# Performance work log

Measured on AMD Instinct MI355X. Metric: run time of the kernel, lower is better.

The kernel has to match this reference:

```python
import jax, jax.numpy as jnp
import numpy as np

N_NODES = 50000
N_EDGES = 800000
IN_CH, HID, OUT_CH = 3, 64, 768
NEG_SLOPE = 0.01  # torch LeakyReLU default
BN_EPS = 1e-5


def _gcn_conv(x, edge_index, W, b):
    # PyG GCNConv: add self-loops, symmetric degree normalization, scatter-add.
    n = x.shape[0]
    loops = jnp.arange(n, dtype=edge_index.dtype)
    src = jnp.concatenate([edge_index[0], loops])
    dst = jnp.concatenate([edge_index[1], loops])
    deg = jax.ops.segment_sum(jnp.ones(src.shape[0], x.dtype), dst, num_segments=n)
    dinv = jnp.where(deg > 0, jax.lax.rsqrt(deg), 0.0)
    norm = dinv[src] * dinv[dst]                      # [E+N]
    h = x @ W                                          # [N, out]
    msg = h[src] * norm[:, None]                       # gather + edge scale
    return jax.ops.segment_sum(msg, dst, num_segments=n) + b


def _block(x, edge_index, W, b, gamma, beta):
    h = _gcn_conv(x, edge_index, W, b)
    h = jnp.where(h >= 0, h, NEG_SLOPE * h)            # LeakyReLU
    mean = h.mean(axis=0)
    var = h.var(axis=0)                                # biased, as torch BN train
    h = (h - mean) * jax.lax.rsqrt(var + BN_EPS) * gamma + beta
    return h                                           # dropout: identity (eval)


def _glorot(key, fan_in, fan_out):
    s = np.sqrt(6.0 / (fan_in + fan_out)).astype(np.float32)
    return jax.random.uniform(key, (fan_in, fan_out), jnp.float32, -s, s)


def setup_inputs() -> dict:
    key = jax.random.key(0)
    ks = jax.random.split(key, 8)
    x = jax.random.normal(ks[0], (N_NODES, IN_CH), jnp.float32)
    edge_index = jax.random.randint(ks[1], (2, N_EDGES), 0, N_NODES, jnp.int64)
    inp = {"x": x, "edge_index": edge_index}
    inp["W1"] = _glorot(ks[2], IN_CH, HID)
    inp["b1"] = jnp.zeros((HID,), jnp.float32)
    inp["g1"] = jnp.ones((HID,), jnp.float32)
    inp["be1"] = jnp.zeros((HID,), jnp.float32)
    inp["W2"] = _glorot(ks[3], HID, HID)
    inp["b2"] = jnp.zeros((HID,), jnp.float32)
    inp["g2"] = jnp.ones((HID,), jnp.float32)
    inp["be2"] = jnp.zeros((HID,), jnp.float32)
    inp["W3"] = _glorot(ks[4], HID, HID)
    inp["b3"] = jnp.zeros((HID,), jnp.float32)
    inp["g3"] = jnp.ones((HID,), jnp.float32)
    inp["be3"] = jnp.zeros((HID,), jnp.float32)
    inp["Wmu"] = _glorot(ks[5], HID, OUT_CH)
    inp["bmu"] = jnp.zeros((OUT_CH,), jnp.float32)
    inp["Wls"] = _glorot(ks[6], HID, OUT_CH)
    inp["bls"] = jnp.zeros((OUT_CH,), jnp.float32)
    return inp


def reference(x, edge_index, W1, b1, g1, be1, W2, b2, g2, be2, W3, b3, g3, be3, Wmu, bmu, Wls, bls):
    h = _block(x, edge_index, W1, b1, g1, be1)
    h = _block(h, edge_index, W2, b2, g2, be2)
    h = _block(h, edge_index, W3, b3, g3, be3)
    mu = _gcn_conv(h, edge_index, Wmu, bmu)
    logstd = _gcn_conv(h, edge_index, Wls, bls)
    return (mu, logstd)
```

## Files before the change

### kernel.cpp

```cpp
#include <hip/hip_runtime.h>
#include <cstddef>


#define NEG_SLOPE 0.01f
#define BN_EPS 1e-5f

typedef unsigned short u16;
typedef __attribute__((ext_vector_type(8))) short bf16x8;
typedef __attribute__((ext_vector_type(4))) float f32x4;

__device__ __forceinline__ unsigned bf16_rne(float x) {
  unsigned u = __float_as_uint(x);
  return (u + 0x7fffu + ((u >> 16) & 1u)) >> 16;
}

__global__ __launch_bounds__(256) void init_k(int* __restrict__ cnt,
                                              float* __restrict__ bns, int N) {
  int i = blockIdx.x * 256 + threadIdx.x;
  if (i < N) cnt[i] = 0;
  if (i < 384) bns[i] = 0.0f;
}

__global__ __launch_bounds__(256) void hist_k(const int* __restrict__ dst,
                                              int* __restrict__ cnt, int E) {
  int e = blockIdx.x * 256 + threadIdx.x;
  if (e < E) atomicAdd(&cnt[dst[e]], 1);
}

__global__ __launch_bounds__(1024) void scanA(const int* __restrict__ cnt,
                                              int* __restrict__ pre,
                                              int* __restrict__ bsum, int N) {
  __shared__ int sh[1024];
  const int t = threadIdx.x;
  const int i = blockIdx.x * 1024 + t;
  int c = (i < N) ? cnt[i] : 0;
  sh[t] = c;
  __syncthreads();
  for (int off = 1; off < 1024; off <<= 1) {
    int v = (t >= off) ? sh[t - off] : 0;
    __syncthreads();
    sh[t] += v;
    __syncthreads();
  }
  if (i < N) pre[i] = sh[t] - c;
  if (t == 1023) bsum[blockIdx.x] = sh[t];
}

__global__ __launch_bounds__(64) void scanB(int* __restrict__ bsum, int nb) {
  int t = threadIdx.x;
  int orig = (t < nb) ? bsum[t] : 0;
  int v = orig;
#pragma unroll
  for (int off = 1; off < 64; off <<= 1) {
    int u = __shfl_up(v, off);
    if (t >= off) v += u;
  }
  if (t < nb) bsum[t] = v - orig;
}

__global__ __launch_bounds__(256) void scanC(const int* __restrict__ cnt,
                                             int* __restrict__ rowptr,
                                             int* __restrict__ cursor,
                                             const int* __restrict__ bsum,
                                             float* __restrict__ dinv,
                                             int N, int E) {
  int i = blockIdx.x * 256 + threadIdx.x;
  if (i < N) {
    int rp = rowptr[i] + bsum[i >> 10];
    rowptr[i] = rp;
    cursor[i] = rp;
    dinv[i] = rsqrtf((float)(cnt[i] + 1));
  }
  if (i == 0) rowptr[N] = E;
}

__global__ __launch_bounds__(256) void fill_k(const int* __restrict__ src,
                                              const int* __restrict__ dst,
                                              int* __restrict__ cursor,
                                              int* __restrict__ eidx, int E) {
  int e = blockIdx.x * 256 + threadIdx.x;
  if (e >= E) return;
  int p = atomicAdd(&cursor[dst[e]], 1);
  eidx[p] = src[e];
}

__global__ __launch_bounds__(256) void l1_fused(
    const int* __restrict__ rowptr, const int* __restrict__ eidx,
    const float* __restrict__ x, const float* __restrict__ dinv,
    const float* __restrict__ W1, const float* __restrict__ b1,
    float* __restrict__ Z, float* __restrict__ q, float* __restrict__ bns, int N) {
  const int t = threadIdx.x, lane = t & 63, wid = t >> 6;
  const int gw = blockIdx.x * 4 + wid;
  const int nw = gridDim.x * 4;
  const float w0 = W1[lane], w1 = W1[64 + lane], w2 = W1[128 + lane];
  const float bb = b1[lane];
  float s1 = 0.f, s2 = 0.f;
  for (int node = gw; node < N; node += nw) {
    int beg = rowptr[node], end = rowptr[node + 1];
    float a0 = 0.f, a1 = 0.f, a2 = 0.f, aq = 0.f;
    for (int e = beg + lane; e < end; e += 64) {
      int s = eidx[e];
      float dv = dinv[s];
      a0 += x[s * 3] * dv;
      a1 += x[s * 3 + 1] * dv;
      a2 += x[s * 3 + 2] * dv;
      aq += dv;
    }
#pragma unroll
    for (int off = 32; off; off >>= 1) {
      a0 += __shfl_xor(a0, off);
      a1 += __shfl_xor(a1, off);
      a2 += __shfl_xor(a2, off);
      aq += __shfl_xor(aq, off);
    }
    float dv = dinv[node];
    a0 += x[node * 3] * dv;
    a1 += x[node * 3 + 1] * dv;
    a2 += x[node * 3 + 2] * dv;
    aq += dv;
    float u = dv * (a0 * w0 + a1 * w1 + a2 * w2) + bb;
    float o = u >= 0.f ? u : NEG_SLOPE * u;
    Z[(size_t)node * 64 + lane] = o * dv;
    s1 += o;
    s2 += o * o;
    if (lane == 0) q[node] = aq;
  }
  __shared__ float red[8][64];
  red[wid][lane] = s1;
  red[4 + wid][lane] = s2;
  __syncthreads();
  if (t < 64) {
    atomicAdd(&bns[t], red[0][t] + red[1][t] + red[2][t] + red[3][t]);
    atomicAdd(&bns[64 + t], red[4][t] + red[5][t] + red[6][t] + red[7][t]);
  }
}

__global__ __launch_bounds__(256) void gather64(const int* __restrict__ rowptr,
                                                const int* __restrict__ eidx,
                                                const float* __restrict__ Z,
                                                float* __restrict__ G, int N) {
  int node = blockIdx.x * 4 + (threadIdx.x >> 6);
  if (node >= N) return;
  int lane = threadIdx.x & 63;
  int slot = lane >> 4;
  int c4 = (lane & 15) << 2;
  int beg = rowptr[node], end = rowptr[node + 1];
  float ax = 0.f, ay = 0.f, az = 0.f, aw = 0.f;
  int e = beg + slot;
  for (; e + 4 < end; e += 8) {
    int s0 = eidx[e], s1 = eidx[e + 4];
    float4 v0 = *(const float4*)(Z + (size_t)s0 * 64 + c4);
    float4 v1 = *(const float4*)(Z + (size_t)s1 * 64 + c4);
    ax += v0.x + v1.x;
    ay += v0.y + v1.y;
    az += v0.z + v1.z;
    aw += v0.w + v1.w;
  }
  if (e < end) {
    int s0 = eidx[e];
    float4 v0 = *(const float4*)(Z + (size_t)s0 * 64 + c4);
    ax += v0.x; ay += v0.y; az += v0.z; aw += v0.w;
  }
#pragma unroll
  for (int off = 16; off < 64; off <<= 1) {
    ax += __shfl_xor(ax, off);
    ay += __shfl_xor(ay, off);
    az += __shfl_xor(az, off);
    aw += __shfl_xor(aw, off);
  }
  if (slot == 0) {
    float4 self = *(const float4*)(Z + (size_t)node * 64 + c4);
    float4 o = make_float4(ax + self.x, ay + self.y, az + self.z, aw + self.w);
    *(float4*)(G + (size_t)node * 64 + c4) = o;
  }
}

__global__ __launch_bounds__(256) void gather64h(const int* __restrict__ rowptr,
                                                 const int* __restrict__ eidx,
                                                 const float* __restrict__ Z,
                                                 u16* __restrict__ Ghi,
                                                 u16* __restrict__ Glo, int N) {
  int node = blockIdx.x * 4 + (threadIdx.x >> 6);
  if (node >= N) return;
  int lane = threadIdx.x & 63;
  int slot = lane >> 4;
  int c4 = (lane & 15) << 2;
  int beg = rowptr[node], end = rowptr[node + 1];
  float ax = 0.f, ay = 0.f, az = 0.f, aw = 0.f;
  int e = beg + slot;
  for (; e + 4 < end; e += 8) {
    int s0 = eidx[e], s1 = eidx[e + 4];
    float4 v0 = *(const float4*)(Z + (size_t)s0 * 64 + c4);
    float4 v1 = *(const float4*)(Z + (size_t)s1 * 64 + c4);
    ax += v0.x + v1.x;
    ay += v0.y + v1.y;
    az += v0.z + v1.z;
    aw += v0.w + v1.w;
  }
  if (e < end) {
    int s0 = eidx[e];
    float4 v0 = *(const float4*)(Z + (size_t)s0 * 64 + c4);
    ax += v0.x; ay += v0.y; az += v0.z; aw += v0.w;
  }
#pragma unroll
  for (int off = 16; off < 64; off <<= 1) {
    ax += __shfl_xor(ax, off);
    ay += __shfl_xor(ay, off);
    az += __shfl_xor(az, off);
    aw += __shfl_xor(aw, off);
  }
  if (slot == 0) {
    float4 self = *(const float4*)(Z + (size_t)node * 64 + c4);
    float o0 = ax + self.x, o1 = ay + self.y, o2 = az + self.z, o3 = aw + self.w;
    unsigned h0 = bf16_rne(o0), h1 = bf16_rne(o1), h2 = bf16_rne(o2), h3 = bf16_rne(o3);
    unsigned l0 = bf16_rne(o0 - __uint_as_float(h0 << 16));
    unsigned l1 = bf16_rne(o1 - __uint_as_float(h1 << 16));
    unsigned l2 = bf16_rne(o2 - __uint_as_float(h2 << 16));
    unsigned l3 = bf16_rne(o3 - __uint_as_float(h3 << 16));
    uint2 hv = make_uint2(h0 | (h1 << 16), h2 | (h3 << 16));
    uint2 lv = make_uint2(l0 | (l1 << 16), l2 | (l3 << 16));
    *(uint2*)(Ghi + (size_t)node * 64 + c4) = hv;
    *(uint2*)(Glo + (size_t)node * 64 + c4) = lv;
  }
}

__global__ __launch_bounds__(256) void prep_small(
    const float* __restrict__ bns, const float* __restrict__ g,
    const float* __restrict__ be, const float* __restrict__ W,
    float* __restrict__ Wc, float* __restrict__ cx, float invN) {
  __shared__ float sc[64], sh[64], part[4][64];
  int t = threadIdx.x;
  if (t < 64) {
    float mean = bns[t] * invN;
    float var = bns[64 + t] * invN - mean * mean;
    float s = g[t] * rsqrtf(var + BN_EPS);
    sc[t] = s;
    sh[t] = be[t] - mean * s;
  }
  __syncthreads();
  int c = t & 63, kq = t >> 6;
  float p = 0.f;
  for (int k = kq * 16; k < kq * 16 + 16; ++k) {
    float w = W[k * 64 + c];
    Wc[k * 64 + c] = sc[k] * w;
    p += sh[k] * w;
  }
  part[kq][c] = p;
  __syncthreads();
  if (t < 64) cx[t] = part[0][t] + part[1][t] + part[2][t] + part[3][t];
}

__global__ __launch_bounds__(256) void prep_head(
    const float* __restrict__ bns, const float* __restrict__ g,
    const float* __restrict__ be, const float* __restrict__ Wmu,
    const float* __restrict__ Wls, u16* __restrict__ Bh, u16* __restrict__ Bl,
    float* __restrict__ cmu, float* __restrict__ cls, float invN) {
  __shared__ float sc[64], sh[64], part[2][128];
  int t = threadIdx.x;
  if (t < 64) {
    float mean = bns[t] * invN;
    float var = bns[64 + t] * invN - mean * mean;
    float s = g[t] * rsqrtf(var + BN_EPS);
    sc[t] = s;
    sh[t] = be[t] - mean * s;
  }
  __syncthreads();
  int blk = blockIdx.x;
  int head = blk >= 6 ? 1 : 0;
  int cc = head ? blk - 6 : blk;
  int c0 = cc * 128;
  const float* W = head ? Wls : Wmu;
  float* cx = head ? cls : cmu;
  int cl = t & 127, kh = t >> 7;
  int c = c0 + cl;
  int ct = cl >> 4, jc = cl & 15;
  size_t base = (size_t)(head * 6 + cc) * 2 * 8 * 64 * 8;
  float p = 0.f;
  for (int k = kh * 32; k < kh * 32 + 32; ++k) {
    float w = W[(size_t)k * 768 + c];
    float wc = sc[k] * w;
    p += sh[k] * w;
    unsigned hi = bf16_rne(wc);
    unsigned lo = bf16_rne(wc - __uint_as_float(hi << 16));
    int lane = ((k >> 3) & 3) * 16 + jc;
    size_t idx = base + (((size_t)kh * 8 + ct) * 64 + lane) * 8 + (k & 7);
    Bh[idx] = (u16)hi;
    Bl[idx] = (u16)lo;
  }
  part[kh][cl] = p;
  __syncthreads();
  if (t < 128) cx[c0 + t] = part[0][t] + part[1][t];
}

__global__ __launch_bounds__(256, 4) void gemm_bnq(
    const float* __restrict__ G, const float* __restrict__ dinv,
    const float* __restrict__ q, const float* __restrict__ Wc,
    const float* __restrict__ cx, const float* __restrict__ b,
    float* __restrict__ Z, float* __restrict__ bns, int N) {
  __shared__ __align__(16) float P[64][68];
  __shared__ __align__(16) float Ws[64][64];
  const int t = threadIdx.x;
  const int r0 = blockIdx.x * 64;

  for (int i = t; i < 1024; i += 256) {
    int r = i >> 4, k4 = (i & 15) << 2, gr = r0 + r;
    float4 v = make_float4(0.f, 0.f, 0.f, 0.f);
    if (gr < N) v = *(const float4*)(G + (size_t)gr * 64 + k4);
    *(float4*)&P[r][k4] = v;
  }
  for (int i = t; i < 4096; i += 256) Ws[i >> 6][i & 63] = Wc[i];
  __syncthreads();

  const int tr = t >> 4, tc4 = (t & 15) << 2;
  float acc[4][4] = {};
#pragma unroll 8
  for (int k = 0; k < 64; ++k) {
    float4 w = *(const float4*)&Ws[k][tc4];
#pragma unroll
    for (int i = 0; i < 4; ++i) {
      float a = P[tr + 16 * i][k];
      acc[i][0] += a * w.x;
      acc[i][1] += a * w.y;
      acc[i][2] += a * w.z;
      acc[i][3] += a * w.w;
    }
  }

  float s1[4] = {0.f, 0.f, 0.f, 0.f}, s2[4] = {0.f, 0.f, 0.f, 0.f};
  float4 bb = *(const float4*)(b + tc4);
  float4 cc = *(const float4*)(cx + tc4);
#pragma unroll
  for (int i = 0; i < 4; ++i) {
    int r = r0 + tr + 16 * i;
    if (r < N) {
      float dv = dinv[r];
      float dq = dv * q[r];
      float u0 = acc[i][0] * dv + dq * cc.x + bb.x;
      float u1 = acc[i][1] * dv + dq * cc.y + bb.y;
      float u2 = acc[i][2] * dv + dq * cc.z + bb.z;
      float u3 = acc[i][3] * dv + dq * cc.w + bb.w;
      float o0 = u0 >= 0.f ? u0 : NEG_SLOPE * u0;
      float o1 = u1 >= 0.f ? u1 : NEG_SLOPE * u1;
      float o2 = u2 >= 0.f ? u2 : NEG_SLOPE * u2;
      float o3 = u3 >= 0.f ? u3 : NEG_SLOPE * u3;
      float4 z = make_float4(o0 * dv, o1 * dv, o2 * dv, o3 * dv);
      *(float4*)(Z + (size_t)r * 64 + tc4) = z;
      s1[0] += o0; s2[0] += o0 * o0;
      s1[1] += o1; s2[1] += o1 * o1;
      s1[2] += o2; s2[2] += o2 * o2;
      s1[3] += o3; s2[3] += o3 * o3;
    }
  }
  __syncthreads();
  float (*red1)[64] = (float(*)[64]) & Ws[0][0];
  float (*red2)[64] = (float(*)[64]) & Ws[16][0];
#pragma unroll
  for (int j = 0; j < 4; ++j) {
    red1[tr][tc4 + j] = s1[j];
    red2[tr][tc4 + j] = s2[j];
  }
  __syncthreads();
  if (t < 64) {
    float a1 = 0.f, a2 = 0.f;
#pragma unroll
    for (int i = 0; i < 16; ++i) {
      a1 += red1[i][t];
      a2 += red2[i][t];
    }
    atomicAdd(&bns[t], a1);
    atomicAdd(&bns[64 + t], a2);
  }
}

__global__ __launch_bounds__(256) void head_mfma(
    const u16* __restrict__ Ghi, const u16* __restrict__ Glo,
    const float* __restrict__ dinv, const float* __restrict__ q,
    const u16* __restrict__ Bh, const u16* __restrict__ Bl,
    const float* __restrict__ cmu, const float* __restrict__ bmu,
    const float* __restrict__ cls, const float* __restrict__ bls,
    float* __restrict__ OUT, int N) {
  const int t = threadIdx.x;
  const int w = t >> 6, l = t & 63;
  const int r0 = blockIdx.x * 64 + w * 16;
  const int yy = blockIdx.y;
  const int head = (yy >= 6) ? 1 : 0;
  const int cc = head ? yy - 6 : yy;
  const int c0 = cc * 128;
  const float* cx = head ? cls : cmu;
  const float* bb = head ? bls : bmu;
  float* O = OUT + (head ? (size_t)N * 768 : 0);

  int arow = r0 + (l & 15);
  if (arow >= N) arow = N - 1;
  const u16* gh = Ghi + (size_t)arow * 64 + ((l >> 4) << 3);
  const u16* gl = Glo + (size_t)arow * 64 + ((l >> 4) << 3);
  const bf16x8 ah0 = *(const bf16x8*)gh;
  const bf16x8 ah1 = *(const bf16x8*)(gh + 32);
  const bf16x8 al0 = *(const bf16x8*)gl;
  const bf16x8 al1 = *(const bf16x8*)(gl + 32);

  const size_t base = (size_t)(head * 6 + cc) * 2 * 8 * 64 * 8;
  const u16* bhp = Bh + base;
  const u16* blp = Bl + base;

  f32x4 acc[8];
#pragma unroll
  for (int ct = 0; ct < 8; ++ct) {
    const bf16x8 bh0 = *(const bf16x8*)(bhp + (((size_t)ct) * 64 + l) * 8);
    const bf16x8 bh1 = *(const bf16x8*)(bhp + (((size_t)(8 + ct)) * 64 + l) * 8);
    const bf16x8 bl0 = *(const bf16x8*)(blp + (((size_t)ct) * 64 + l) * 8);
    const bf16x8 bl1 = *(const bf16x8*)(blp + (((size_t)(8 + ct)) * 64 + l) * 8);
    f32x4 a = {0.f, 0.f, 0.f, 0.f};
    a = __builtin_amdgcn_mfma_f32_16x16x32_bf16(ah0, bh0, a, 0, 0, 0);
    a = __builtin_amdgcn_mfma_f32_16x16x32_bf16(ah1, bh1, a, 0, 0, 0);
    a = __builtin_amdgcn_mfma_f32_16x16x32_bf16(ah0, bl0, a, 0, 0, 0);
    a = __builtin_amdgcn_mfma_f32_16x16x32_bf16(ah1, bl1, a, 0, 0, 0);
    a = __builtin_amdgcn_mfma_f32_16x16x32_bf16(al0, bh0, a, 0, 0, 0);
    a = __builtin_amdgcn_mfma_f32_16x16x32_bf16(al1, bh1, a, 0, 0, 0);
    acc[ct] = a;
  }

  const int jc = l & 15;
  const int rbase = r0 + ((l >> 4) << 2);
  float dv[4], dq[4];
#pragma unroll
  for (int r = 0; r < 4; ++r) {
    int row = rbase + r;
    int rc = row < N ? row : N - 1;
    dv[r] = dinv[rc];
    dq[r] = dv[r] * q[rc];
  }
#pragma unroll
  for (int ct = 0; ct < 8; ++ct) {
    int col = c0 + ct * 16 + jc;
    float cxv = cx[col], bbv = bb[col];
#pragma unroll
    for (int r = 0; r < 4; ++r) {
      int row = rbase + r;
      if (row < N)
        O[(size_t)row * 768 + col] = acc[ct][r] * dv[r] + dq[r] * cxv + bbv;
    }
  }
}

extern "C" void kernel_launch(void* const* d_in, const int* in_sizes, int n_in,
                              void* d_out, int out_size, void* d_ws, size_t ws_size,
                              hipStream_t stream) {
  const float* x   = (const float*)d_in[0];
  const int*   ei  = (const int*)d_in[1];
  const float* W1  = (const float*)d_in[2];
  const float* b1  = (const float*)d_in[3];
  const float* g1  = (const float*)d_in[4];
  const float* be1 = (const float*)d_in[5];
  const float* W2  = (const float*)d_in[6];
  const float* b2  = (const float*)d_in[7];
  const float* g2  = (const float*)d_in[8];
  const float* be2 = (const float*)d_in[9];
  const float* W3  = (const float*)d_in[10];
  const float* b3  = (const float*)d_in[11];
  const float* g3  = (const float*)d_in[12];
  const float* be3 = (const float*)d_in[13];
  const float* Wmu = (const float*)d_in[14];
  const float* bmu = (const float*)d_in[15];
  const float* Wls = (const float*)d_in[16];
  const float* bls = (const float*)d_in[17];

  const int N = in_sizes[0] / 3;
  const int E = in_sizes[1] / 2;
  const int* src = ei;
  const int* dst = ei + E;
  float* out = (float*)d_out;

  char* ws = (char*)d_ws;
  size_t o = 0;
  float* dinv = (float*)(ws + o); o += (size_t)N * 4;
  float* qv   = (float*)(ws + o); o += (size_t)N * 4;
  float* bns  = (float*)(ws + o); o += 384 * 4;
  float* W2c  = (float*)(ws + o); o += 4096 * 4;
  float* c2   = (float*)(ws + o); o += 64 * 4;
  float* W3c  = (float*)(ws + o); o += 4096 * 4;
  float* c3   = (float*)(ws + o); o += 64 * 4;
  u16* Bh     = (u16*)(ws + o);   o += (size_t)12 * 2 * 8 * 64 * 8 * 2;
  u16* Bl     = (u16*)(ws + o);   o += (size_t)12 * 2 * 8 * 64 * 8 * 2;
  float* cmu  = (float*)(ws + o); o += 768 * 4;
  float* cls  = (float*)(ws + o); o += 768 * 4;
  u16* Ghi    = (u16*)(ws + o);   o += (size_t)N * 64 * 2;
  u16* Glo    = (u16*)(ws + o);   o += (size_t)N * 64 * 2;
  int* cnt    = (int*)(ws + o);   o += (size_t)N * 4;
  int* rowptr = (int*)(ws + o);   o += ((size_t)N + 1) * 4;
  int* cursor = (int*)(ws + o);   o += (size_t)N * 4;
  int* bsum   = (int*)(ws + o);   o += 64 * 4;
  int* eidx   = (int*)(ws + o);   o += (size_t)E * 4;
  float* B0   = (float*)(ws + o); o += (size_t)N * 64 * 4;
  float* B1   = (float*)(ws + o); o += (size_t)N * 64 * 4;

  const float invN = 1.0f / (float)N;
  int nbN = (N + 255) / 256;
  int nbE = (E + 255) / 256;
  int gb  = (N + 63) / 64;
  int wb  = (N + 3) / 4;
  int sbA = (N + 1023) / 1024;

  init_k<<<nbN, 256, 0, stream>>>(cnt, bns, N);
  hist_k<<<nbE, 256, 0, stream>>>(dst, cnt, E);
  scanA<<<sbA, 1024, 0, stream>>>(cnt, rowptr, bsum, N);
  scanB<<<1, 64, 0, stream>>>(bsum, sbA);
  scanC<<<nbN, 256, 0, stream>>>(cnt, rowptr, cursor, bsum, dinv, N, E);
  fill_k<<<nbE, 256, 0, stream>>>(src, dst, cursor, eidx, E);

  l1_fused<<<1024, 256, 0, stream>>>(rowptr, eidx, x, dinv, W1, b1, B0, qv, bns, N);
  prep_small<<<1, 256, 0, stream>>>(bns + 0, g1, be1, W2, W2c, c2, invN);

  gather64<<<wb, 256, 0, stream>>>(rowptr, eidx, B0, B1, N);
  gemm_bnq<<<gb, 256, 0, stream>>>(B1, dinv, qv, W2c, c2, b2, B0, bns + 128, N);
  prep_small<<<1, 256, 0, stream>>>(bns + 128, g2, be2, W3, W3c, c3, invN);

  gather64<<<wb, 256, 0, stream>>>(rowptr, eidx, B0, B1, N);
  gemm_bnq<<<gb, 256, 0, stream>>>(B1, dinv, qv, W3c, c3, b3, B0, bns + 256, N);
  prep_head<<<12, 256, 0, stream>>>(bns + 256, g3, be3, Wmu, Wls, Bh, Bl, cmu, cls, invN);

  gather64h<<<wb, 256, 0, stream>>>(rowptr, eidx, B0, Ghi, Glo, N);
  dim3 hgrid(gb, 12);
  head_mfma<<<hgrid, 256, 0, stream>>>(Ghi, Glo, dinv, qv, Bh, Bl,
                                       cmu, bmu, cls, bls, out, N);
}
```

Baseline: 427.6 us.

## Persist head GEMM blocks with register-resident weights and swapped MFMA operands

Turns the output-head MFMA kernel into a persistent grid of 64x12 blocks. Each block loads its B-weight fragments into registers once and loops over row tiles. The MFMA operands are swapped so each lane holds four consecutive output columns, which allows float4 stores and vectorized bias/c loads instead of scalar strided stores. This amortizes weight loads and improves store coalescing for the 2x50000x768 output. The cost is much higher register pressure from 32 held bf16x8 values, and a grid of only 768 blocks may limit occupancy.

```diff
diff --git a/kernel.cpp b/kernel.cpp
--- a/kernel.cpp
+++ b/kernel.cpp
@@ -372,16 +372,15 @@
   }
 }
 
-__global__ __launch_bounds__(256) void head_mfma(
+__global__ __launch_bounds__(256) void head_mfma2(
     const u16* __restrict__ Ghi, const u16* __restrict__ Glo,
     const float* __restrict__ dinv, const float* __restrict__ q,
     const u16* __restrict__ Bh, const u16* __restrict__ Bl,
     const float* __restrict__ cmu, const float* __restrict__ bmu,
     const float* __restrict__ cls, const float* __restrict__ bls,
-    float* __restrict__ OUT, int N) {
+    float* __restrict__ OUT, int N, int ntiles) {
   const int t = threadIdx.x;
   const int w = t >> 6, l = t & 63;
-  const int r0 = blockIdx.x * 64 + w * 16;
   const int yy = blockIdx.y;
   const int head = (yy >= 6) ? 1 : 0;
   const int cc = head ? yy - 6 : yy;
@@ -390,55 +389,50 @@
   const float* bb = head ? bls : bmu;
   float* O = OUT + (head ? (size_t)N * 768 : 0);
 
-  int arow = r0 + (l & 15);
-  if (arow >= N) arow = N - 1;
-  const u16* gh = Ghi + (size_t)arow * 64 + ((l >> 4) << 3);
-  const u16* gl = Glo + (size_t)arow * 64 + ((l >> 4) << 3);
-  const bf16x8 ah0 = *(const bf16x8*)gh;
-  const bf16x8 ah1 = *(const bf16x8*)(gh + 32);
-  const bf16x8 al0 = *(const bf16x8*)gl;
-  const bf16x8 al1 = *(const bf16x8*)(gl + 32);
-
   const size_t base = (size_t)(head * 6 + cc) * 2 * 8 * 64 * 8;
   const u16* bhp = Bh + base;
   const u16* blp = Bl + base;
-
-  f32x4 acc[8];
+  bf16x8 wh[8][2], wl[8][2];
 #pragma unroll
   for (int ct = 0; ct < 8; ++ct) {
-    const bf16x8 bh0 = *(const bf16x8*)(bhp + (((size_t)ct) * 64 + l) * 8);
-    const bf16x8 bh1 = *(const bf16x8*)(bhp + (((size_t)(8 + ct)) * 64 + l) * 8);
-    const bf16x8 bl0 = *(const bf16x8*)(blp + (((size_t)ct) * 64 + l) * 8);
-    const bf16x8 bl1 = *(const bf16x8*)(blp + (((size_t)(8 + ct)) * 64 + l) * 8);
-    f32x4 a = {0.f, 0.f, 0.f, 0.f};
-    a = __builtin_amdgcn_mfma_f32_16x16x32_bf16(ah0, bh0, a, 0, 0, 0);
-    a = __builtin_amdgcn_mfma_f32_16x16x32_bf16(ah1, bh1, a, 0, 0, 0);
-    a = __builtin_amdgcn_mfma_f32_16x16x32_bf16(ah0, bl0, a, 0, 0, 0);
-    a = __builtin_amdgcn_mfma_f32_16x16x32_bf16(ah1, bl1, a, 0, 0, 0);
-    a = __builtin_amdgcn_mfma_f32_16x16x32_bf16(al0, bh0, a, 0, 0, 0);
-    a = __builtin_amdgcn_mfma_f32_16x16x32_bf16(al1, bh1, a, 0, 0, 0);
-    acc[ct] = a;
-  }
-
-  const int jc = l & 15;
-  const int rbase = r0 + ((l >> 4) << 2);
-  float dv[4], dq[4];
-#pragma unroll
-  for (int r = 0; r < 4; ++r) {
-    int row = rbase + r;
-    int rc = row < N ? row : N - 1;
-    dv[r] = dinv[rc];
-    dq[r] = dv[r] * q[rc];
-  }
-#pragma unroll
-  for (int ct = 0; ct < 8; ++ct) {
-    int col = c0 + ct * 16 + jc;
-    float cxv = cx[col], bbv = bb[col];
-#pragma unroll
-    for (int r = 0; r < 4; ++r) {
-      int row = rbase + r;
-      if (row < N)
-        O[(size_t)row * 768 + col] = acc[ct][r] * dv[r] + dq[r] * cxv + bbv;
+    wh[ct][0] = *(const bf16x8*)(bhp + (((size_t)ct) * 64 + l) * 8);
+    wh[ct][1] = *(const bf16x8*)(bhp + (((size_t)(8 + ct)) * 64 + l) * 8);
+    wl[ct][0] = *(const bf16x8*)(blp + (((size_t)ct) * 64 + l) * 8);
+    wl[ct][1] = *(const bf16x8*)(blp + (((size_t)(8 + ct)) * 64 + l) * 8);
+  }
+
+  const int colb = c0 + ((l >> 4) << 2);
+  for (int tile = blockIdx.x; tile < ntiles; tile += gridDim.x) {
+    const int grow = tile * 64 + w * 16 + (l & 15);
+    const int gc = grow < N ? grow : N - 1;
+    const u16* gh = Ghi + (size_t)gc * 64 + ((l >> 4) << 3);
+    const u16* gl = Glo + (size_t)gc * 64 + ((l >> 4) << 3);
+    const bf16x8 gh0 = *(const bf16x8*)gh;
+    const bf16x8 gh1 = *(const bf16x8*)(gh + 32);
+    const bf16x8 gl0 = *(const bf16x8*)gl;
+    const bf16x8 gl1 = *(const bf16x8*)(gl + 32);
+    const float dv = dinv[gc];
+    const float dq = dv * q[gc];
+
+#pragma unroll
+    for (int ct = 0; ct < 8; ++ct) {
+      f32x4 a = {0.f, 0.f, 0.f, 0.f};
+      a = __builtin_amdgcn_mfma_f32_16x16x32_bf16(wh[ct][0], gh0, a, 0, 0, 0);
+      a = __builtin_amdgcn_mfma_f32_16x16x32_bf16(wh[ct][1], gh1, a, 0, 0, 0);
+      a = __builtin_amdgcn_mfma_f32_16x16x32_bf16(wl[ct][0], gh0, a, 0, 0, 0);
+      a = __builtin_amdgcn_mfma_f32_16x16x32_bf16(wl[ct][1], gh1, a, 0, 0, 0);
+      a = __builtin_amdgcn_mfma_f32_16x16x32_bf16(wh[ct][0], gl0, a, 0, 0, 0);
+      a = __builtin_amdgcn_mfma_f32_16x16x32_bf16(wh[ct][1], gl1, a, 0, 0, 0);
+      if (grow < N) {
+        int col = colb + ct * 16;
+        float4 cxv = *(const float4*)(cx + col);
+        float4 bbv = *(const float4*)(bb + col);
+        float4 o = make_float4(a[0] * dv + dq * cxv.x + bbv.x,
+                               a[1] * dv + dq * cxv.y + bbv.y,
+                               a[2] * dv + dq * cxv.z + bbv.z,
+                               a[3] * dv + dq * cxv.w + bbv.w);
+        *(float4*)(O + (size_t)grow * 768 + col) = o;
+      }
     }
   }
 }
@@ -520,7 +514,7 @@
   prep_head<<<12, 256, 0, stream>>>(bns + 256, g3, be3, Wmu, Wls, Bh, Bl, cmu, cls, invN);
 
   gather64h<<<wb, 256, 0, stream>>>(rowptr, eidx, B0, Ghi, Glo, N);
-  dim3 hgrid(gb, 12);
-  head_mfma<<<hgrid, 256, 0, stream>>>(Ghi, Glo, dinv, qv, Bh, Bl,
-                                       cmu, bmu, cls, bls, out, N);
-}
+  dim3 hgrid(64, 12);
+  head_mfma2<<<hgrid, 256, 0, stream>>>(Ghi, Glo, dinv, qv, Bh, Bl,
+                                        cmu, bmu, cls, bls, out, N, gb);
+}
```

Measured after the change: 418.8 us. -2.1%, faster.
